# Kernel optimization log

Measured on AMD Instinct MI355X. Metric: run time of the kernel, lower is better.

Reference implementation:

```python
import jax, jax.numpy as jnp
import numpy as np

N = 100000    # nodes
E = 1600000   # directed edges
EPS = 1e-5    # BatchNorm eps (torch default)


def _bn(x, g, b, rm, rv):
    # BatchNorm1d in eval mode: running stats
    return (x - rm) * jax.lax.rsqrt(rv + EPS) * g + b


def _gcn(x, W, b, src, dst, norm):
    # PyG GCNConv: linear transform then symmetric-normalized scatter-add
    h = x @ W                                  # [N, d_out]
    msg = h[src] * norm[:, None]               # [E+N, d_out] gather + scale
    return jax.ops.segment_sum(msg, dst, num_segments=N) + b


def setup_inputs():
    ks = iter(jax.random.split(jax.random.key(0), 64))
    f32 = jnp.float32
    def w(shape, s=0.05):
        return jax.random.normal(next(ks), shape, dtype=f32) * s
    def rvar(n):
        return jax.random.uniform(next(ks), (n,), f32, 0.5, 1.5)
    inp = {}
    inp['x'] = jax.random.normal(next(ks), (N, 42), f32)
    inp['edge_index'] = jax.random.randint(next(ks), (2, E), 0, N, dtype=jnp.int32)
    dims = [(42, 128), (128, 256), (256, 128), (128, 64)]
    for i, (di, do) in enumerate(dims, 1):
        inp[f'W{i}'] = w((di, do))
        inp[f'b{i}'] = jnp.zeros((do,), f32)
        inp[f'g{i}'] = jnp.ones((do,), f32)
        inp[f'be{i}'] = jnp.zeros((do,), f32)
        inp[f'rm{i}'] = w((do,), 0.1)
        inp[f'rv{i}'] = rvar(do)
    cdims = [(64, 64), (64, 32)]
    for i, (di, do) in enumerate(cdims, 1):
        inp[f'cW{i}'] = w((di, do))
        inp[f'cb{i}'] = jnp.zeros((do,), f32)
        inp[f'cg{i}'] = jnp.ones((do,), f32)
        inp[f'cbe{i}'] = jnp.zeros((do,), f32)
        inp[f'crm{i}'] = w((do,), 0.1)
        inp[f'crv{i}'] = rvar(do)
    inp['cW3'] = w((32, 2))
    inp['cb3'] = jnp.zeros((2,), f32)
    return inp


def reference(x, edge_index,
              W1, b1, g1, be1, rm1, rv1,
              W2, b2, g2, be2, rm2, rv2,
              W3, b3, g3, be3, rm3, rv3,
              W4, b4, g4, be4, rm4, rv4,
              cW1, cb1, cg1, cbe1, crm1, crv1,
              cW2, cb2, cg2, cbe2, crm2, crv2,
              cW3, cb3):
    # add self-loops, compute D^{-1/2}(A+I)D^{-1/2} edge weights
    loop = jnp.arange(N, dtype=edge_index.dtype)
    src = jnp.concatenate([edge_index[0], loop])
    dst = jnp.concatenate([edge_index[1], loop])
    deg = jax.ops.segment_sum(jnp.ones_like(src, dtype=x.dtype), dst, num_segments=N)
    dis = jax.lax.rsqrt(deg)                   # deg >= 1 due to self-loops
    norm = dis[src] * dis[dst]                 # [E+N]
    # 4 stacked GCNConv + BN + ReLU (dropout = identity in eval mode)
    h = jax.nn.relu(_bn(_gcn(x, W1, b1, src, dst, norm), g1, be1, rm1, rv1))
    h = jax.nn.relu(_bn(_gcn(h, W2, b2, src, dst, norm), g2, be2, rm2, rv2))
    h = jax.nn.relu(_bn(_gcn(h, W3, b3, src, dst, norm), g3, be3, rm3, rv3))
    h = jax.nn.relu(_bn(_gcn(h, W4, b4, src, dst, norm), g4, be4, rm4, rv4))
    # classifier: Linear -> ReLU -> BN (x2) -> Linear
    h = _bn(jax.nn.relu(h @ cW1 + cb1), cg1, cbe1, crm1, crv1)
    h = _bn(jax.nn.relu(h @ cW2 + cb2), cg2, cbe2, crm2, crv2)
    return h @ cW3 + cb3
```

## Files before the change

### kernel.cpp

```cpp
#include <hip/hip_runtime.h>

#define EPS 1e-5f
#define CAP 64
#define NXCD 8
#define ECHUNK 2048

typedef __attribute__((ext_vector_type(8))) short short8v;
typedef __attribute__((ext_vector_type(4))) float f32x4;

__device__ __forceinline__ unsigned short f2bf(float f) {
    union { float f; unsigned int u; } v; v.f = f;
    unsigned int r = v.u + 0x7fffu + ((v.u >> 16) & 1u);
    return (unsigned short)(r >> 16);
}
__device__ __forceinline__ float bf2f(unsigned short h) {
    union { unsigned int u; float f; } v; v.u = ((unsigned int)h) << 16;
    return v.f;
}

__global__ __launch_bounds__(256) void ell_fill(const int* __restrict__ src, const int* __restrict__ dst,
                                                int* __restrict__ cnt, int* __restrict__ ell,
                                                int E, int nper) {
    const int xcd = blockIdx.x & (NXCD - 1);
    const int chunk = blockIdx.x >> 3;
    const int dLo = xcd * nper;
    const int dHi = dLo + nper;
    const int base = chunk * ECHUNK;
#pragma unroll
    for (int it = 0; it < ECHUNK / 256; ++it) {
        int i = base + it * 256 + threadIdx.x;
        if (i < E) {
            int d = dst[i];
            if (d >= dLo && d < dHi) {
                int s = src[i];
                int pos = atomicAdd(&cnt[d], 1);
                if (pos < CAP) ell[((size_t)d << 6) + pos] = s;
            }
        }
    }
}

__global__ __launch_bounds__(256) void calc_dis(const int* __restrict__ cnt, float* __restrict__ dis, int n) {
    int i = blockIdx.x * 256 + threadIdx.x;
    if (i < n) dis[i] = rsqrtf((float)cnt[i] + 1.0f);
}

__global__ __launch_bounds__(256) void prep(const float* __restrict__ x, const float* __restrict__ dis,
                                            unsigned short* __restrict__ xs1,
                                            const float* __restrict__ W1, float* __restrict__ W1p,
                                            const float* __restrict__ W2, unsigned short* __restrict__ w2h,
                                            unsigned short* __restrict__ w2l,
                                            const float* __restrict__ W3, unsigned short* __restrict__ w3h,
                                            unsigned short* __restrict__ w3l,
                                            const float* __restrict__ W4, unsigned short* __restrict__ w4h,
                                            unsigned short* __restrict__ w4l,
                                            int n, int nbx) {
    int bi = blockIdx.x;
    if (bi < nbx) {
        int gid = bi * 256 + threadIdx.x;
        int nd = gid / 48, c = gid - nd * 48;
        if (nd < n) {
            float v = (c < 42) ? x[(size_t)nd * 42 + c] * dis[nd] : 0.0f;
            xs1[(size_t)nd * 48 + c] = f2bf(v);
        }
        return;
    }
    bi -= nbx;
    if (bi < 24) {
        int i = bi * 256 + threadIdx.x;
        int k = i >> 7;
        W1p[i] = (k < 42) ? W1[i] : 0.0f;
        return;
    }
    bi -= 24;
    if (bi < 128) {
        int i = bi * 256 + threadIdx.x;
        int c = i >> 7, k = i & 127;
        float w = W2[(size_t)k * 256 + c];
        unsigned short h = f2bf(w);
        w2h[i] = h; w2l[i] = f2bf(w - bf2f(h));
        return;
    }
    bi -= 128;
    if (bi < 128) {
        int i = bi * 256 + threadIdx.x;
        int c = i >> 8, k = i & 255;
        float w = W3[(size_t)k * 128 + c];
        unsigned short h = f2bf(w);
        w3h[i] = h; w3l[i] = f2bf(w - bf2f(h));
        return;
    }
    bi -= 128;
    {
        int i = bi * 256 + threadIdx.x;
        int c = i >> 7, k = i & 127;
        float w = W4[(size_t)k * 64 + c];
        unsigned short h = f2bf(w);
        w4h[i] = h; w4l[i] = f2bf(w - bf2f(h));
        return;
    }
}

template<int D, int FUSE>
__global__ __launch_bounds__(256) void agg_bf(const unsigned short* __restrict__ x, const float* __restrict__ dis,
                                              const int* __restrict__ cnt, const int* __restrict__ ell,
                                              const float* __restrict__ b, const float* __restrict__ g,
                                              const float* __restrict__ be, const float* __restrict__ rm,
                                              const float* __restrict__ rv,
                                              float* __restrict__ out, int n) {
    constexpr int CPE = D / 8;
    int gid = blockIdx.x * 256 + threadIdx.x;
    int nd = gid / CPE, c = gid - nd * CPE;
    if (nd >= n) return;

    float acc[8];
    {
        short8v v = *reinterpret_cast<const short8v*>(x + (size_t)nd * D + c * 8);
#pragma unroll
        for (int j = 0; j < 8; ++j) acc[j] = bf2f((unsigned short)v[j]);
    }
    int deg = cnt[nd];
    deg = (deg < CAP) ? deg : CAP;
    const int* row = ell + ((size_t)nd << 6);
    int i = 0;
    for (; i + 2 <= deg; i += 2) {
        int s0 = row[i], s1 = row[i + 1];
        short8v v0 = *reinterpret_cast<const short8v*>(x + (size_t)s0 * D + c * 8);
        short8v v1 = *reinterpret_cast<const short8v*>(x + (size_t)s1 * D + c * 8);
#pragma unroll
        for (int j = 0; j < 8; ++j) acc[j] += bf2f((unsigned short)v0[j]);
#pragma unroll
        for (int j = 0; j < 8; ++j) acc[j] += bf2f((unsigned short)v1[j]);
    }
    if (i < deg) {
        int s0 = row[i];
        short8v v = *reinterpret_cast<const short8v*>(x + (size_t)s0 * D + c * 8);
#pragma unroll
        for (int j = 0; j < 8; ++j) acc[j] += bf2f((unsigned short)v[j]);
    }

    float dn = dis[nd];
#pragma unroll
    for (int j = 0; j < 8; ++j) acc[j] *= dn;

    if (FUSE == 1) {
#pragma unroll
        for (int j = 0; j < 8; ++j) {
            int col = c * 8 + j;
            float sv = g[col] * rsqrtf(rv[col] + EPS);
            float bb = b[col] * sv + (be[col] - rm[col] * sv);
            acc[j] = fmaxf(acc[j] + bb, 0.0f);
        }
    }

    float4 o0, o1;
    o0.x = acc[0]; o0.y = acc[1]; o0.z = acc[2]; o0.w = acc[3];
    o1.x = acc[4]; o1.y = acc[5]; o1.z = acc[6]; o1.w = acc[7];
    float* op = out + (size_t)nd * D + c * 8;
    *reinterpret_cast<float4*>(op) = o0;
    *reinterpret_cast<float4*>(op + 4) = o1;
}

template<int K, int DOUT, int MODE, int OUTBF, int RS>
__global__ __launch_bounds__(256) void gemm_mfma(const float* __restrict__ X,
                                                 const unsigned short* __restrict__ Wh,
                                                 const unsigned short* __restrict__ Wl,
                                                 const float* __restrict__ b, const float* __restrict__ g,
                                                 const float* __restrict__ be, const float* __restrict__ rm,
                                                 const float* __restrict__ rv, const float* __restrict__ dis,
                                                 void* __restrict__ outv, int n) {
    constexpr int BN = (DOUT < 128) ? DOUT : 128;
    constexpr int NT = BN / 16;
    constexpr int KSTEPS = K / 32;
    constexpr int LDA = 40;
    __shared__ unsigned short xh[64][LDA], xl[64][LDA];
    __shared__ unsigned short wh[BN][LDA], wl[BN][LDA];

    const int tid = threadIdx.x;
    const int wave = tid >> 6, lane = tid & 63;
    const int row0 = blockIdx.x * 64;
    const int col0 = blockIdx.y * BN;
    const int r_l = lane & 15;
    const int k_l = (lane >> 4) * 8;

    f32x4 acc[NT];
#pragma unroll
    for (int t = 0; t < NT; ++t) acc[t] = (f32x4){0.f, 0.f, 0.f, 0.f};

    for (int ks = 0; ks < KSTEPS; ++ks) {
        const int k0 = ks * 32;
        for (int i = tid; i < 64 * 8; i += 256) {
            int m = i >> 3, q = i & 7;
            int rr = row0 + m;
            float4 v = (rr < n) ? *reinterpret_cast<const float4*>(X + (size_t)rr * K + k0 + q * 4)
                                : make_float4(0.f, 0.f, 0.f, 0.f);
            unsigned short h0 = f2bf(v.x), h1 = f2bf(v.y), h2 = f2bf(v.z), h3 = f2bf(v.w);
            unsigned short l0 = f2bf(v.x - bf2f(h0)), l1 = f2bf(v.y - bf2f(h1));
            unsigned short l2 = f2bf(v.z - bf2f(h2)), l3 = f2bf(v.w - bf2f(h3));
            uint2 ph = make_uint2((unsigned)h0 | ((unsigned)h1 << 16), (unsigned)h2 | ((unsigned)h3 << 16));
            uint2 pl = make_uint2((unsigned)l0 | ((unsigned)l1 << 16), (unsigned)l2 | ((unsigned)l3 << 16));
            *reinterpret_cast<uint2*>(&xh[m][q * 4]) = ph;
            *reinterpret_cast<uint2*>(&xl[m][q * 4]) = pl;
        }
        for (int i = tid; i < BN * 4; i += 256) {
            int cc = i >> 2, q = i & 3;
            size_t goff = (size_t)(col0 + cc) * K + k0 + q * 8;
            *reinterpret_cast<uint4*>(&wh[cc][q * 8]) = *reinterpret_cast<const uint4*>(Wh + goff);
            *reinterpret_cast<uint4*>(&wl[cc][q * 8]) = *reinterpret_cast<const uint4*>(Wl + goff);
        }
        __syncthreads();

        short8v ah = *reinterpret_cast<const short8v*>(&xh[wave * 16 + r_l][k_l]);
        short8v al = *reinterpret_cast<const short8v*>(&xl[wave * 16 + r_l][k_l]);
#pragma unroll
        for (int t = 0; t < NT; ++t) {
            short8v bh = *reinterpret_cast<const short8v*>(&wh[t * 16 + r_l][k_l]);
            short8v bl = *reinterpret_cast<const short8v*>(&wl[t * 16 + r_l][k_l]);
            acc[t] = __builtin_amdgcn_mfma_f32_16x16x32_bf16(ah, bh, acc[t], 0, 0, 0);
            acc[t] = __builtin_amdgcn_mfma_f32_16x16x32_bf16(al, bh, acc[t], 0, 0, 0);
            acc[t] = __builtin_amdgcn_mfma_f32_16x16x32_bf16(ah, bl, acc[t], 0, 0, 0);
        }
        __syncthreads();
    }

    const int orow = row0 + wave * 16 + (lane >> 4) * 4;
    float dsc[4];
#pragma unroll
    for (int r = 0; r < 4; ++r)
        dsc[r] = (RS && orow + r < n) ? dis[orow + r] : 1.0f;

#pragma unroll
    for (int t = 0; t < NT; ++t) {
        int col = col0 + t * 16 + r_l;
        float s, tt, bias;
        if (MODE == 0 || MODE == 2) {
            float sv = g[col] * rsqrtf(rv[col] + EPS);
            s = sv; tt = be[col] - rm[col] * sv; bias = b[col];
        } else {
            s = g[col] * rsqrtf(rv[col] + EPS); tt = 0.f; bias = 0.f;
        }
#pragma unroll
        for (int r = 0; r < 4; ++r) {
            int rr = orow + r;
            if (rr < n) {
                float z = acc[t][r];
                if (MODE == 0)      { z = (z + bias) * s + tt; z = fmaxf(z, 0.0f); }
                else if (MODE == 1) { z = z * s; }
                else                { z = fmaxf(z + bias, 0.0f) * s + tt; }
                if (RS) z *= dsc[r];
                if (OUTBF) ((unsigned short*)outv)[(size_t)rr * DOUT + col] = f2bf(z);
                else       ((float*)outv)[(size_t)rr * DOUT + col] = z;
            }
        }
    }
}

template<int K, int DOUT, int MODE, int OUTBF, int RS>
__global__ __launch_bounds__(256) void gemm_tile(const float* __restrict__ X, const float* __restrict__ W,
                                                 const float* __restrict__ b, const float* __restrict__ g,
                                                 const float* __restrict__ be, const float* __restrict__ rm,
                                                 const float* __restrict__ rv, const float* __restrict__ dis,
                                                 void* __restrict__ outv, int n) {
    constexpr int TM = 8;
    constexpr int TN = (DOUT >= 64) ? 8 : 4;
    constexpr int BN = (DOUT < 128) ? DOUT : 128;
    constexpr int BM = 256 * TM * TN / BN;
    constexpr int KT = (K % 32 == 0) ? 32 : K;
    constexpr int NTN = BN / TN;
    static_assert((BM / TM) * NTN == 256, "thread mapping");

    __shared__ float xs[BM][KT + 1];
    __shared__ float ws[KT][BN];

    const int tid = threadIdx.x;
    const int tn_idx = tid % NTN;
    const int tm_idx = tid / NTN;
    const int row0 = blockIdx.x * BM;
    const int col0 = blockIdx.y * BN;

    float acc[TM][TN];
#pragma unroll
    for (int i = 0; i < TM; ++i)
#pragma unroll
        for (int j = 0; j < TN; ++j) acc[i][j] = 0.0f;

    for (int k0 = 0; k0 < K; k0 += KT) {
        for (int i = tid; i < BM * KT / 4; i += 256) {
            int m = i / (KT / 4), kq = i - m * (KT / 4);
            int k = kq * 4;
            int rr = row0 + m;
            float4 v = (rr < n) ? *reinterpret_cast<const float4*>(X + (size_t)rr * K + k0 + k)
                                : make_float4(0.f, 0.f, 0.f, 0.f);
            xs[m][k + 0] = v.x; xs[m][k + 1] = v.y; xs[m][k + 2] = v.z; xs[m][k + 3] = v.w;
        }
        for (int i = tid; i < KT * BN / 4; i += 256) {
            int k = i / (BN / 4), cq = i - k * (BN / 4);
            float4 wv = *reinterpret_cast<const float4*>(W + (size_t)(k0 + k) * DOUT + col0 + cq * 4);
            *reinterpret_cast<float4*>(&ws[k][cq * 4]) = wv;
        }
        __syncthreads();

#pragma unroll 2
        for (int k = 0; k < KT; ++k) {
            float av[TM], bv[TN];
#pragma unroll
            for (int i = 0; i < TM; ++i) av[i] = xs[tm_idx * TM + i][k];
#pragma unroll
            for (int j = 0; j < TN; j += 4)
                *reinterpret_cast<float4*>(&bv[j]) = *reinterpret_cast<const float4*>(&ws[k][tn_idx * TN + j]);
#pragma unroll
            for (int i = 0; i < TM; ++i)
#pragma unroll
                for (int j = 0; j < TN; ++j)
                    acc[i][j] = fmaf(av[i], bv[j], acc[i][j]);
        }
        __syncthreads();
    }

    float s[TN], t[TN], bias[TN];
#pragma unroll
    for (int j = 0; j < TN; ++j) {
        int col = col0 + tn_idx * TN + j;
        if (MODE == 0 || MODE == 2) {
            float sv = g[col] * rsqrtf(rv[col] + EPS);
            s[j] = sv; t[j] = be[col] - rm[col] * sv; bias[j] = b[col];
        } else {
            s[j] = g[col] * rsqrtf(rv[col] + EPS); t[j] = 0.f; bias[j] = 0.f;
        }
    }

#pragma unroll
    for (int i = 0; i < TM; ++i) {
        int rr = row0 + tm_idx * TM + i;
        if (rr < n) {
            float dsc = RS ? dis[rr] : 1.0f;
            float o[TN];
#pragma unroll
            for (int j = 0; j < TN; ++j) {
                float z = acc[i][j];
                if (MODE == 0)      { z = (z + bias[j]) * s[j] + t[j]; z = fmaxf(z, 0.0f); }
                else if (MODE == 1) { z = z * s[j]; }
                else                { z = fmaxf(z + bias[j], 0.0f) * s[j] + t[j]; }
                if (RS) z *= dsc;
                o[j] = z;
            }
            if (OUTBF) {
                unsigned short* op = (unsigned short*)outv + (size_t)rr * DOUT + col0 + tn_idx * TN;
                unsigned int pk[TN / 2];
#pragma unroll
                for (int j2 = 0; j2 < TN / 2; ++j2)
                    pk[j2] = (unsigned)f2bf(o[2 * j2]) | ((unsigned)f2bf(o[2 * j2 + 1]) << 16);
#pragma unroll
                for (int j2 = 0; j2 < TN / 2; ++j2)
                    *reinterpret_cast<unsigned int*>(op + 2 * j2) = pk[j2];
            } else {
                float* op = (float*)outv + (size_t)rr * DOUT + col0 + tn_idx * TN;
#pragma unroll
                for (int j = 0; j < TN; j += 4)
                    *reinterpret_cast<float4*>(op + j) = *reinterpret_cast<const float4*>(&o[j]);
            }
        }
    }
}

__global__ __launch_bounds__(256) void classifier_fused(
    const float* __restrict__ X,
    const float* __restrict__ cW1, const float* __restrict__ cb1,
    const float* __restrict__ cg1, const float* __restrict__ cbe1,
    const float* __restrict__ crm1, const float* __restrict__ crv1,
    const float* __restrict__ cW2, const float* __restrict__ cb2,
    const float* __restrict__ cg2, const float* __restrict__ cbe2,
    const float* __restrict__ crm2, const float* __restrict__ crv2,
    const float* __restrict__ cW3, const float* __restrict__ cb3,
    float* __restrict__ out, int n)
{
    __shared__ float xs[64][65];
    __shared__ float h1[64][65];
    __shared__ float h2[64][33];
    const int tid = threadIdx.x;
    const int row0 = blockIdx.x * 64;

    for (int i = tid; i < 64 * 16; i += 256) {
        int r = i >> 4, cq = i & 15;
        int rr = row0 + r;
        float4 v = (rr < n) ? *reinterpret_cast<const float4*>(X + (size_t)rr * 64 + cq * 4)
                            : make_float4(0.f, 0.f, 0.f, 0.f);
        xs[r][cq * 4 + 0] = v.x; xs[r][cq * 4 + 1] = v.y;
        xs[r][cq * 4 + 2] = v.z; xs[r][cq * 4 + 3] = v.w;
    }
    __syncthreads();

    {
        const int col = tid & 63;
        const int rg  = tid >> 6;
        float sv = cg1[col] * rsqrtf(crv1[col] + EPS);
        float tt = cbe1[col] - crm1[col] * sv;
        float bias = cb1[col];
        float accv[16];
#pragma unroll
        for (int r = 0; r < 16; ++r) accv[r] = 0.f;
#pragma unroll 4
        for (int k = 0; k < 64; ++k) {
            float w = cW1[k * 64 + col];
#pragma unroll
            for (int r = 0; r < 16; ++r)
                accv[r] = fmaf(xs[rg * 16 + r][k], w, accv[r]);
        }
#pragma unroll
        for (int r = 0; r < 16; ++r)
            h1[rg * 16 + r][col] = fmaxf(accv[r] + bias, 0.f) * sv + tt;
    }
    __syncthreads();

    {
        const int col = tid & 31;
        const int rg  = tid >> 5;
        float sv = cg2[col] * rsqrtf(crv2[col] + EPS);
        float tt = cbe2[col] - crm2[col] * sv;
        float bias = cb2[col];
        float accv[8];
#pragma unroll
        for (int r = 0; r < 8; ++r) accv[r] = 0.f;
#pragma unroll 4
        for (int k = 0; k < 64; ++k) {
            float w = cW2[k * 32 + col];
#pragma unroll
            for (int r = 0; r < 8; ++r)
                accv[r] = fmaf(h1[rg * 8 + r][k], w, accv[r]);
        }
#pragma unroll
        for (int r = 0; r < 8; ++r)
            h2[rg * 8 + r][col] = fmaxf(accv[r] + bias, 0.f) * sv + tt;
    }
    __syncthreads();

    if (tid < 64) {
        int rr = row0 + tid;
        if (rr < n) {
            float a0 = 0.f, a1 = 0.f;
#pragma unroll
            for (int k = 0; k < 32; ++k) {
                float h = h2[tid][k];
                a0 = fmaf(h, cW3[k * 2 + 0], a0);
                a1 = fmaf(h, cW3[k * 2 + 1], a1);
            }
            out[(size_t)rr * 2 + 0] = a0 + cb3[0];
            out[(size_t)rr * 2 + 1] = a1 + cb3[1];
        }
    }
}


extern "C" void kernel_launch(void* const* d_in, const int* in_sizes, int n_in,
                              void* d_out, int out_size, void* d_ws, size_t ws_size,
                              hipStream_t stream) {
    const float* x  = (const float*)d_in[0];
    const int*   ei = (const int*)d_in[1];
    const int E = in_sizes[1] / 2;
    const int n = in_sizes[0] / 42;
    const int* src = ei;
    const int* dst = ei + E;

    const float *W1 = (const float*)d_in[2],  *b1 = (const float*)d_in[3],  *g1 = (const float*)d_in[4],
                *be1 = (const float*)d_in[5], *rm1 = (const float*)d_in[6], *rv1 = (const float*)d_in[7];
    const float *W2 = (const float*)d_in[8],  *b2 = (const float*)d_in[9],  *g2 = (const float*)d_in[10],
                *be2 = (const float*)d_in[11], *rm2 = (const float*)d_in[12], *rv2 = (const float*)d_in[13];
    const float *W3 = (const float*)d_in[14], *b3 = (const float*)d_in[15], *g3 = (const float*)d_in[16],
                *be3 = (const float*)d_in[17], *rm3 = (const float*)d_in[18], *rv3 = (const float*)d_in[19];
    const float *W4 = (const float*)d_in[20], *b4 = (const float*)d_in[21], *g4 = (const float*)d_in[22],
                *be4 = (const float*)d_in[23], *rm4 = (const float*)d_in[24], *rv4 = (const float*)d_in[25];
    const float *cW1 = (const float*)d_in[26], *cb1 = (const float*)d_in[27], *cg1 = (const float*)d_in[28],
                *cbe1 = (const float*)d_in[29], *crm1 = (const float*)d_in[30], *crv1 = (const float*)d_in[31];
    const float *cW2 = (const float*)d_in[32], *cb2 = (const float*)d_in[33], *cg2 = (const float*)d_in[34],
                *cbe2 = (const float*)d_in[35], *crm2 = (const float*)d_in[36], *crv2 = (const float*)d_in[37];
    const float *cW3 = (const float*)d_in[38], *cb3 = (const float*)d_in[39];

    int*   ell    = (int*)d_ws;
    float* bufA   = (float*)(ell + (size_t)n * CAP);
    float* bufB   = bufA + (size_t)n * 128;
    unsigned short* hbf = (unsigned short*)(bufB + (size_t)n * 256);
    unsigned short* xs1 = hbf + (size_t)n * 128;
    float* dis    = (float*)(xs1 + (size_t)n * 48);
    int*   cnt    = (int*)(dis + n);
    float* W1p    = (float*)(cnt + n);
    unsigned short* w2h = (unsigned short*)(W1p + 48 * 128);
    unsigned short* w2l = w2h + 256 * 128;
    unsigned short* w3h = w2l + 256 * 128;
    unsigned short* w3l = w3h + 128 * 256;
    unsigned short* w4h = w3l + 128 * 256;
    unsigned short* w4l = w4h + 64 * 128;

    dim3 blk(256);
    auto nb = [](long total) { return dim3((unsigned)((total + 255) / 256)); };
    const int nbx = (int)(((long)n * 48 + 255) / 256);
    const int nper = (n + NXCD - 1) / NXCD;
    const int nchunk = (E + ECHUNK - 1) / ECHUNK;
    const float* nul = nullptr;

    hipMemsetAsync(cnt, 0, (size_t)n * sizeof(int), stream);
    ell_fill<<<dim3(nchunk * NXCD), blk, 0, stream>>>(src, dst, cnt, ell, E, nper);
    calc_dis<<<nb(n), blk, 0, stream>>>(cnt, dis, n);
    prep<<<dim3(nbx + 24 + 128 + 128 + 32), blk, 0, stream>>>(x, dis, xs1, W1, W1p,
                                                              W2, w2h, w2l, W3, w3h, w3l,
                                                              W4, w4h, w4l, n, nbx);

    agg_bf<48, 0><<<nb((long)n * 6), blk, 0, stream>>>(xs1, dis, cnt, ell, nul, nul, nul, nul, nul, bufA, n);
    gemm_tile<48, 128, 0, 1, 1><<<dim3((n + 127) / 128, 1), blk, 0, stream>>>(bufA, W1p, b1, g1, be1, rm1, rv1, dis, (void*)hbf, n);

    agg_bf<128, 0><<<nb((long)n * 16), blk, 0, stream>>>(hbf, dis, cnt, ell, nul, nul, nul, nul, nul, bufA, n);
    gemm_mfma<128, 256, 0, 0, 0><<<dim3((n + 63) / 64, 2), blk, 0, stream>>>(bufA, w2h, w2l, b2, g2, be2, rm2, rv2, nul, (void*)bufB, n);

    gemm_mfma<256, 128, 1, 1, 1><<<dim3((n + 63) / 64, 1), blk, 0, stream>>>(bufB, w3h, w3l, b3, g3, be3, rm3, rv3, dis, (void*)hbf, n);
    agg_bf<128, 1><<<nb((long)n * 16), blk, 0, stream>>>(hbf, dis, cnt, ell, b3, g3, be3, rm3, rv3, bufA, n);

    gemm_mfma<128, 64, 1, 1, 1><<<dim3((n + 63) / 64, 1), blk, 0, stream>>>(bufA, w4h, w4l, b4, g4, be4, rm4, rv4, dis, (void*)hbf, n);
    agg_bf<64, 1><<<nb((long)n * 8), blk, 0, stream>>>(hbf, dis, cnt, ell, b4, g4, be4, rm4, rv4, bufB, n);

    classifier_fused<<<dim3((n + 63) / 64), blk, 0, stream>>>(bufB, cW1, cb1, cg1, cbe1, crm1, crv1,
                                                              cW2, cb2, cg2, cbe2, crm2, crv2,
                                                              cW3, cb3, (float*)d_out, n);
}
```

Measured before the change: 494.5 us.

## Store all intermediate activations in bf16 and drop low-part activation MFMA

Aggregation outputs and GEMM inputs/outputs are now stored as bf16 instead of fp32, which roughly halves the inter-kernel activation traffic. The GEMMs load bf16 activations directly and skip the activation low-part split, cutting one of three MFMAs per tile. The first-layer scalar FMA GEMM is replaced by the MFMA path with padded, split W1. The calc_dis kernel is removed and rsqrt(cnt+1) is recomputed inline. The trade is extra rounding error from bf16 activations against less memory traffic and compute.

```diff
diff --git a/kernel.cpp b/kernel.cpp
--- a/kernel.cpp
+++ b/kernel.cpp
@@ -40,14 +40,10 @@
     }
 }
 
-__global__ __launch_bounds__(256) void calc_dis(const int* __restrict__ cnt, float* __restrict__ dis, int n) {
-    int i = blockIdx.x * 256 + threadIdx.x;
-    if (i < n) dis[i] = rsqrtf((float)cnt[i] + 1.0f);
-}
-
-__global__ __launch_bounds__(256) void prep(const float* __restrict__ x, const float* __restrict__ dis,
+__global__ __launch_bounds__(256) void prep(const float* __restrict__ x, const int* __restrict__ cnt,
                                             unsigned short* __restrict__ xs1,
-                                            const float* __restrict__ W1, float* __restrict__ W1p,
+                                            const float* __restrict__ W1, unsigned short* __restrict__ w1h,
+                                            unsigned short* __restrict__ w1l,
                                             const float* __restrict__ W2, unsigned short* __restrict__ w2h,
                                             unsigned short* __restrict__ w2l,
                                             const float* __restrict__ W3, unsigned short* __restrict__ w3h,
@@ -60,19 +56,22 @@
         int gid = bi * 256 + threadIdx.x;
         int nd = gid / 48, c = gid - nd * 48;
         if (nd < n) {
-            float v = (c < 42) ? x[(size_t)nd * 42 + c] * dis[nd] : 0.0f;
+            float v = 0.0f;
+            if (c < 42) v = x[(size_t)nd * 42 + c] * rsqrtf((float)cnt[nd] + 1.0f);
             xs1[(size_t)nd * 48 + c] = f2bf(v);
         }
         return;
     }
     bi -= nbx;
-    if (bi < 24) {
+    if (bi < 32) {
         int i = bi * 256 + threadIdx.x;
-        int k = i >> 7;
-        W1p[i] = (k < 42) ? W1[i] : 0.0f;
+        int c = i >> 6, k = i & 63;
+        float w = (k < 42) ? W1[(size_t)k * 128 + c] : 0.0f;
+        unsigned short h = f2bf(w);
+        w1h[i] = h; w1l[i] = f2bf(w - bf2f(h));
         return;
     }
-    bi -= 24;
+    bi -= 32;
     if (bi < 128) {
         int i = bi * 256 + threadIdx.x;
         int c = i >> 7, k = i & 127;
@@ -102,12 +101,12 @@
 }
 
 template<int D, int FUSE>
-__global__ __launch_bounds__(256) void agg_bf(const unsigned short* __restrict__ x, const float* __restrict__ dis,
+__global__ __launch_bounds__(256) void agg_bf(const unsigned short* __restrict__ x,
                                               const int* __restrict__ cnt, const int* __restrict__ ell,
                                               const float* __restrict__ b, const float* __restrict__ g,
                                               const float* __restrict__ be, const float* __restrict__ rm,
                                               const float* __restrict__ rv,
-                                              float* __restrict__ out, int n) {
+                                              unsigned short* __restrict__ out, int n) {
     constexpr int CPE = D / 8;
     int gid = blockIdx.x * 256 + threadIdx.x;
     int nd = gid / CPE, c = gid - nd * CPE;
@@ -119,8 +118,9 @@
 #pragma unroll
         for (int j = 0; j < 8; ++j) acc[j] = bf2f((unsigned short)v[j]);
     }
-    int deg = cnt[nd];
-    deg = (deg < CAP) ? deg : CAP;
+    const int cv = cnt[nd];
+    const int deg = (cv < CAP) ? cv : CAP;
+    const float dn = rsqrtf((float)cv + 1.0f);
     const int* row = ell + ((size_t)nd << 6);
     int i = 0;
     for (; i + 2 <= deg; i += 2) {
@@ -139,7 +139,6 @@
         for (int j = 0; j < 8; ++j) acc[j] += bf2f((unsigned short)v[j]);
     }
 
-    float dn = dis[nd];
 #pragma unroll
     for (int j = 0; j < 8; ++j) acc[j] *= dn;
 
@@ -153,27 +152,27 @@
         }
     }
 
-    float4 o0, o1;
-    o0.x = acc[0]; o0.y = acc[1]; o0.z = acc[2]; o0.w = acc[3];
-    o1.x = acc[4]; o1.y = acc[5]; o1.z = acc[6]; o1.w = acc[7];
-    float* op = out + (size_t)nd * D + c * 8;
-    *reinterpret_cast<float4*>(op) = o0;
-    *reinterpret_cast<float4*>(op + 4) = o1;
-}
-
-template<int K, int DOUT, int MODE, int OUTBF, int RS>
-__global__ __launch_bounds__(256) void gemm_mfma(const float* __restrict__ X,
-                                                 const unsigned short* __restrict__ Wh,
-                                                 const unsigned short* __restrict__ Wl,
-                                                 const float* __restrict__ b, const float* __restrict__ g,
-                                                 const float* __restrict__ be, const float* __restrict__ rm,
-                                                 const float* __restrict__ rv, const float* __restrict__ dis,
-                                                 void* __restrict__ outv, int n) {
+    uint4 pk;
+    pk.x = (unsigned)f2bf(acc[0]) | ((unsigned)f2bf(acc[1]) << 16);
+    pk.y = (unsigned)f2bf(acc[2]) | ((unsigned)f2bf(acc[3]) << 16);
+    pk.z = (unsigned)f2bf(acc[4]) | ((unsigned)f2bf(acc[5]) << 16);
+    pk.w = (unsigned)f2bf(acc[6]) | ((unsigned)f2bf(acc[7]) << 16);
+    *reinterpret_cast<uint4*>(out + (size_t)nd * D + c * 8) = pk;
+}
+
+template<int KROW, int KPAD, int DOUT, int MODE, int RS>
+__global__ __launch_bounds__(256) void gemm_xbf(const unsigned short* __restrict__ X,
+                                                const unsigned short* __restrict__ Wh,
+                                                const unsigned short* __restrict__ Wl,
+                                                const float* __restrict__ b, const float* __restrict__ g,
+                                                const float* __restrict__ be, const float* __restrict__ rm,
+                                                const float* __restrict__ rv, const int* __restrict__ cnt,
+                                                unsigned short* __restrict__ out, int n) {
     constexpr int BN = (DOUT < 128) ? DOUT : 128;
     constexpr int NT = BN / 16;
-    constexpr int KSTEPS = K / 32;
+    constexpr int KSTEPS = KPAD / 32;
     constexpr int LDA = 40;
-    __shared__ unsigned short xh[64][LDA], xl[64][LDA];
+    __shared__ unsigned short xh[64][LDA];
     __shared__ unsigned short wh[BN][LDA], wl[BN][LDA];
 
     const int tid = threadIdx.x;
@@ -189,35 +188,29 @@
 
     for (int ks = 0; ks < KSTEPS; ++ks) {
         const int k0 = ks * 32;
-        for (int i = tid; i < 64 * 8; i += 256) {
-            int m = i >> 3, q = i & 7;
-            int rr = row0 + m;
-            float4 v = (rr < n) ? *reinterpret_cast<const float4*>(X + (size_t)rr * K + k0 + q * 4)
-                                : make_float4(0.f, 0.f, 0.f, 0.f);
-            unsigned short h0 = f2bf(v.x), h1 = f2bf(v.y), h2 = f2bf(v.z), h3 = f2bf(v.w);
-            unsigned short l0 = f2bf(v.x - bf2f(h0)), l1 = f2bf(v.y - bf2f(h1));
-            unsigned short l2 = f2bf(v.z - bf2f(h2)), l3 = f2bf(v.w - bf2f(h3));
-            uint2 ph = make_uint2((unsigned)h0 | ((unsigned)h1 << 16), (unsigned)h2 | ((unsigned)h3 << 16));
-            uint2 pl = make_uint2((unsigned)l0 | ((unsigned)l1 << 16), (unsigned)l2 | ((unsigned)l3 << 16));
-            *reinterpret_cast<uint2*>(&xh[m][q * 4]) = ph;
-            *reinterpret_cast<uint2*>(&xl[m][q * 4]) = pl;
+        {
+            int i = tid;
+            int m = i >> 2, q = i & 3;
+            int rr = row0 + m, kk = k0 + q * 8;
+            uint4 v = make_uint4(0u, 0u, 0u, 0u);
+            if (rr < n && kk < KROW)
+                v = *reinterpret_cast<const uint4*>(X + (size_t)rr * KROW + kk);
+            *reinterpret_cast<uint4*>(&xh[m][q * 8]) = v;
         }
         for (int i = tid; i < BN * 4; i += 256) {
             int cc = i >> 2, q = i & 3;
-            size_t goff = (size_t)(col0 + cc) * K + k0 + q * 8;
+            size_t goff = (size_t)(col0 + cc) * KPAD + k0 + q * 8;
             *reinterpret_cast<uint4*>(&wh[cc][q * 8]) = *reinterpret_cast<const uint4*>(Wh + goff);
             *reinterpret_cast<uint4*>(&wl[cc][q * 8]) = *reinterpret_cast<const uint4*>(Wl + goff);
         }
         __syncthreads();
 
         short8v ah = *reinterpret_cast<const short8v*>(&xh[wave * 16 + r_l][k_l]);
-        short8v al = *reinterpret_cast<const short8v*>(&xl[wave * 16 + r_l][k_l]);
 #pragma unroll
         for (int t = 0; t < NT; ++t) {
             short8v bh = *reinterpret_cast<const short8v*>(&wh[t * 16 + r_l][k_l]);
             short8v bl = *reinterpret_cast<const short8v*>(&wl[t * 16 + r_l][k_l]);
             acc[t] = __builtin_amdgcn_mfma_f32_16x16x32_bf16(ah, bh, acc[t], 0, 0, 0);
-            acc[t] = __builtin_amdgcn_mfma_f32_16x16x32_bf16(al, bh, acc[t], 0, 0, 0);
             acc[t] = __builtin_amdgcn_mfma_f32_16x16x32_bf16(ah, bl, acc[t], 0, 0, 0);
         }
         __syncthreads();
@@ -227,13 +220,13 @@
     float dsc[4];
 #pragma unroll
     for (int r = 0; r < 4; ++r)
-        dsc[r] = (RS && orow + r < n) ? dis[orow + r] : 1.0f;
+        dsc[r] = (RS && orow + r < n) ? rsqrtf((float)cnt[orow + r] + 1.0f) : 1.0f;
 
 #pragma unroll
     for (int t = 0; t < NT; ++t) {
         int col = col0 + t * 16 + r_l;
         float s, tt, bias;
-        if (MODE == 0 || MODE == 2) {
+        if (MODE == 0) {
             float sv = g[col] * rsqrtf(rv[col] + EPS);
             s = sv; tt = be[col] - rm[col] * sv; bias = b[col];
         } else {
@@ -244,127 +237,17 @@
             int rr = orow + r;
             if (rr < n) {
                 float z = acc[t][r];
-                if (MODE == 0)      { z = (z + bias) * s + tt; z = fmaxf(z, 0.0f); }
-                else if (MODE == 1) { z = z * s; }
-                else                { z = fmaxf(z + bias, 0.0f) * s + tt; }
+                if (MODE == 0) { z = (z + bias) * s + tt; z = fmaxf(z, 0.0f); }
+                else           { z = z * s; }
                 if (RS) z *= dsc[r];
-                if (OUTBF) ((unsigned short*)outv)[(size_t)rr * DOUT + col] = f2bf(z);
-                else       ((float*)outv)[(size_t)rr * DOUT + col] = z;
+                out[(size_t)rr * DOUT + col] = f2bf(z);
             }
         }
     }
 }
 
-template<int K, int DOUT, int MODE, int OUTBF, int RS>
-__global__ __launch_bounds__(256) void gemm_tile(const float* __restrict__ X, const float* __restrict__ W,
-                                                 const float* __restrict__ b, const float* __restrict__ g,
-                                                 const float* __restrict__ be, const float* __restrict__ rm,
-                                                 const float* __restrict__ rv, const float* __restrict__ dis,
-                                                 void* __restrict__ outv, int n) {
-    constexpr int TM = 8;
-    constexpr int TN = (DOUT >= 64) ? 8 : 4;
-    constexpr int BN = (DOUT < 128) ? DOUT : 128;
-    constexpr int BM = 256 * TM * TN / BN;
-    constexpr int KT = (K % 32 == 0) ? 32 : K;
-    constexpr int NTN = BN / TN;
-    static_assert((BM / TM) * NTN == 256, "thread mapping");
-
-    __shared__ float xs[BM][KT + 1];
-    __shared__ float ws[KT][BN];
-
-    const int tid = threadIdx.x;
-    const int tn_idx = tid % NTN;
-    const int tm_idx = tid / NTN;
-    const int row0 = blockIdx.x * BM;
-    const int col0 = blockIdx.y * BN;
-
-    float acc[TM][TN];
-#pragma unroll
-    for (int i = 0; i < TM; ++i)
-#pragma unroll
-        for (int j = 0; j < TN; ++j) acc[i][j] = 0.0f;
-
-    for (int k0 = 0; k0 < K; k0 += KT) {
-        for (int i = tid; i < BM * KT / 4; i += 256) {
-            int m = i / (KT / 4), kq = i - m * (KT / 4);
-            int k = kq * 4;
-            int rr = row0 + m;
-            float4 v = (rr < n) ? *reinterpret_cast<const float4*>(X + (size_t)rr * K + k0 + k)
-                                : make_float4(0.f, 0.f, 0.f, 0.f);
-            xs[m][k + 0] = v.x; xs[m][k + 1] = v.y; xs[m][k + 2] = v.z; xs[m][k + 3] = v.w;
-        }
-        for (int i = tid; i < KT * BN / 4; i += 256) {
-            int k = i / (BN / 4), cq = i - k * (BN / 4);
-            float4 wv = *reinterpret_cast<const float4*>(W + (size_t)(k0 + k) * DOUT + col0 + cq * 4);
-            *reinterpret_cast<float4*>(&ws[k][cq * 4]) = wv;
-        }
-        __syncthreads();
-
-#pragma unroll 2
-        for (int k = 0; k < KT; ++k) {
-            float av[TM], bv[TN];
-#pragma unroll
-            for (int i = 0; i < TM; ++i) av[i] = xs[tm_idx * TM + i][k];
-#pragma unroll
-            for (int j = 0; j < TN; j += 4)
-                *reinterpret_cast<float4*>(&bv[j]) = *reinterpret_cast<const float4*>(&ws[k][tn_idx * TN + j]);
-#pragma unroll
-            for (int i = 0; i < TM; ++i)
-#pragma unroll
-                for (int j = 0; j < TN; ++j)
-                    acc[i][j] = fmaf(av[i], bv[j], acc[i][j]);
-        }
-        __syncthreads();
-    }
-
-    float s[TN], t[TN], bias[TN];
-#pragma unroll
-    for (int j = 0; j < TN; ++j) {
-        int col = col0 + tn_idx * TN + j;
-        if (MODE == 0 || MODE == 2) {
-            float sv = g[col] * rsqrtf(rv[col] + EPS);
-            s[j] = sv; t[j] = be[col] - rm[col] * sv; bias[j] = b[col];
-        } else {
-            s[j] = g[col] * rsqrtf(rv[col] + EPS); t[j] = 0.f; bias[j] = 0.f;
-        }
-    }
-
-#pragma unroll
-    for (int i = 0; i < TM; ++i) {
-        int rr = row0 + tm_idx * TM + i;
-        if (rr < n) {
-            float dsc = RS ? dis[rr] : 1.0f;
-            float o[TN];
-#pragma unroll
-            for (int j = 0; j < TN; ++j) {
-                float z = acc[i][j];
-                if (MODE == 0)      { z = (z + bias[j]) * s[j] + t[j]; z = fmaxf(z, 0.0f); }
-                else if (MODE == 1) { z = z * s[j]; }
-                else                { z = fmaxf(z + bias[j], 0.0f) * s[j] + t[j]; }
-                if (RS) z *= dsc;
-                o[j] = z;
-            }
-            if (OUTBF) {
-                unsigned short* op = (unsigned short*)outv + (size_t)rr * DOUT + col0 + tn_idx * TN;
-                unsigned int pk[TN / 2];
-#pragma unroll
-                for (int j2 = 0; j2 < TN / 2; ++j2)
-                    pk[j2] = (unsigned)f2bf(o[2 * j2]) | ((unsigned)f2bf(o[2 * j2 + 1]) << 16);
-#pragma unroll
-                for (int j2 = 0; j2 < TN / 2; ++j2)
-                    *reinterpret_cast<unsigned int*>(op + 2 * j2) = pk[j2];
-            } else {
-                float* op = (float*)outv + (size_t)rr * DOUT + col0 + tn_idx * TN;
-#pragma unroll
-                for (int j = 0; j < TN; j += 4)
-                    *reinterpret_cast<float4*>(op + j) = *reinterpret_cast<const float4*>(&o[j]);
-            }
-        }
-    }
-}
-
 __global__ __launch_bounds__(256) void classifier_fused(
-    const float* __restrict__ X,
+    const unsigned short* __restrict__ X,
     const float* __restrict__ cW1, const float* __restrict__ cb1,
     const float* __restrict__ cg1, const float* __restrict__ cbe1,
     const float* __restrict__ crm1, const float* __restrict__ crv1,
@@ -380,13 +263,17 @@
     const int tid = threadIdx.x;
     const int row0 = blockIdx.x * 64;
 
-    for (int i = tid; i < 64 * 16; i += 256) {
-        int r = i >> 4, cq = i & 15;
+    for (int i = tid; i < 64 * 8; i += 256) {
+        int r = i >> 3, cq = i & 7;
         int rr = row0 + r;
-        float4 v = (rr < n) ? *reinterpret_cast<const float4*>(X + (size_t)rr * 64 + cq * 4)
-                            : make_float4(0.f, 0.f, 0.f, 0.f);
-        xs[r][cq * 4 + 0] = v.x; xs[r][cq * 4 + 1] = v.y;
-        xs[r][cq * 4 + 2] = v.z; xs[r][cq * 4 + 3] = v.w;
+        if (rr < n) {
+            short8v v = *reinterpret_cast<const short8v*>(X + (size_t)rr * 64 + cq * 8);
+#pragma unroll
+            for (int j = 0; j < 8; ++j) xs[r][cq * 8 + j] = bf2f((unsigned short)v[j]);
+        } else {
+#pragma unroll
+            for (int j = 0; j < 8; ++j) xs[r][cq * 8 + j] = 0.0f;
+        }
     }
     __syncthreads();
 
@@ -475,15 +362,15 @@
                 *cbe2 = (const float*)d_in[35], *crm2 = (const float*)d_in[36], *crv2 = (const float*)d_in[37];
     const float *cW3 = (const float*)d_in[38], *cb3 = (const float*)d_in[39];
 
-    int*   ell    = (int*)d_ws;
-    float* bufA   = (float*)(ell + (size_t)n * CAP);
-    float* bufB   = bufA + (size_t)n * 128;
-    unsigned short* hbf = (unsigned short*)(bufB + (size_t)n * 256);
-    unsigned short* xs1 = hbf + (size_t)n * 128;
-    float* dis    = (float*)(xs1 + (size_t)n * 48);
-    int*   cnt    = (int*)(dis + n);
-    float* W1p    = (float*)(cnt + n);
-    unsigned short* w2h = (unsigned short*)(W1p + 48 * 128);
+    int* ell = (int*)d_ws;
+    unsigned short* P   = (unsigned short*)(ell + (size_t)n * CAP);
+    unsigned short* Q   = P + (size_t)n * 256;
+    unsigned short* R   = Q + (size_t)n * 128;
+    unsigned short* xs1 = R + (size_t)n * 128;
+    int* cnt = (int*)(xs1 + (size_t)n * 48);
+    unsigned short* w1h = (unsigned short*)(cnt + n);
+    unsigned short* w1l = w1h + 128 * 64;
+    unsigned short* w2h = w1l + 128 * 64;
     unsigned short* w2l = w2h + 256 * 128;
     unsigned short* w3h = w2l + 256 * 128;
     unsigned short* w3l = w3h + 128 * 256;
@@ -499,24 +386,23 @@
 
     hipMemsetAsync(cnt, 0, (size_t)n * sizeof(int), stream);
     ell_fill<<<dim3(nchunk * NXCD), blk, 0, stream>>>(src, dst, cnt, ell, E, nper);
-    calc_dis<<<nb(n), blk, 0, stream>>>(cnt, dis, n);
-    prep<<<dim3(nbx + 24 + 128 + 128 + 32), blk, 0, stream>>>(x, dis, xs1, W1, W1p,
-                                                              W2, w2h, w2l, W3, w3h, w3l,
-                                                              W4, w4h, w4l, n, nbx);
-
-    agg_bf<48, 0><<<nb((long)n * 6), blk, 0, stream>>>(xs1, dis, cnt, ell, nul, nul, nul, nul, nul, bufA, n);
-    gemm_tile<48, 128, 0, 1, 1><<<dim3((n + 127) / 128, 1), blk, 0, stream>>>(bufA, W1p, b1, g1, be1, rm1, rv1, dis, (void*)hbf, n);
-
-    agg_bf<128, 0><<<nb((long)n * 16), blk, 0, stream>>>(hbf, dis, cnt, ell, nul, nul, nul, nul, nul, bufA, n);
-    gemm_mfma<128, 256, 0, 0, 0><<<dim3((n + 63) / 64, 2), blk, 0, stream>>>(bufA, w2h, w2l, b2, g2, be2, rm2, rv2, nul, (void*)bufB, n);
-
-    gemm_mfma<256, 128, 1, 1, 1><<<dim3((n + 63) / 64, 1), blk, 0, stream>>>(bufB, w3h, w3l, b3, g3, be3, rm3, rv3, dis, (void*)hbf, n);
-    agg_bf<128, 1><<<nb((long)n * 16), blk, 0, stream>>>(hbf, dis, cnt, ell, b3, g3, be3, rm3, rv3, bufA, n);
-
-    gemm_mfma<128, 64, 1, 1, 1><<<dim3((n + 63) / 64, 1), blk, 0, stream>>>(bufA, w4h, w4l, b4, g4, be4, rm4, rv4, dis, (void*)hbf, n);
-    agg_bf<64, 1><<<nb((long)n * 8), blk, 0, stream>>>(hbf, dis, cnt, ell, b4, g4, be4, rm4, rv4, bufB, n);
-
-    classifier_fused<<<dim3((n + 63) / 64), blk, 0, stream>>>(bufB, cW1, cb1, cg1, cbe1, crm1, crv1,
+    prep<<<dim3(nbx + 32 + 128 + 128 + 32), blk, 0, stream>>>(x, cnt, xs1,
+                                                              W1, w1h, w1l, W2, w2h, w2l,
+                                                              W3, w3h, w3l, W4, w4h, w4l, n, nbx);
+
+    agg_bf<48, 0><<<nb((long)n * 6), blk, 0, stream>>>(xs1, cnt, ell, nul, nul, nul, nul, nul, R, n);
+    gemm_xbf<48, 64, 128, 0, 1><<<dim3((n + 63) / 64, 1), blk, 0, stream>>>(R, w1h, w1l, b1, g1, be1, rm1, rv1, cnt, Q, n);
+
+    agg_bf<128, 0><<<nb((long)n * 16), blk, 0, stream>>>(Q, cnt, ell, nul, nul, nul, nul, nul, R, n);
+    gemm_xbf<128, 128, 256, 0, 0><<<dim3((n + 63) / 64, 2), blk, 0, stream>>>(R, w2h, w2l, b2, g2, be2, rm2, rv2, cnt, P, n);
+
+    gemm_xbf<256, 256, 128, 1, 1><<<dim3((n + 63) / 64, 1), blk, 0, stream>>>(P, w3h, w3l, b3, g3, be3, rm3, rv3, cnt, Q, n);
+    agg_bf<128, 1><<<nb((long)n * 16), blk, 0, stream>>>(Q, cnt, ell, b3, g3, be3, rm3, rv3, R, n);
+
+    gemm_xbf<128, 128, 64, 1, 1><<<dim3((n + 63) / 64, 1), blk, 0, stream>>>(R, w4h, w4l, b4, g4, be4, rm4, rv4, cnt, Q, n);
+    agg_bf<64, 1><<<nb((long)n * 8), blk, 0, stream>>>(Q, cnt, ell, b4, g4, be4, rm4, rv4, R, n);
+
+    classifier_fused<<<dim3((n + 63) / 64), blk, 0, stream>>>(R, cW1, cb1, cg1, cbe1, crm1, crv1,
                                                               cW2, cb2, cg2, cbe2, crm2, crv2,
                                                               cW3, cb3, (float*)d_out, n);
 }
```

Result: faster. 455.2 us (-7.9%).
